# Kernel tuning notes

Measured on AMD Instinct MI355X. Metric: run time of the kernel, lower is better.

## Reference

```python
import jax, jax.numpy as jnp
import numpy as np

N_NODES = 100000
N_EDGES = 1600000
IN_DIM = 128
OUT_DIM = 64


def setup_inputs() -> dict:
    key = jax.random.key(0)
    k1, k2, k3 = jax.random.split(key, 3)
    x = jax.random.normal(k1, (N_NODES, IN_DIM), dtype=jnp.float32)
    edge_index = jax.random.randint(k2, (2, N_EDGES), 0, N_NODES, dtype=jnp.int64)
    W = jax.random.normal(k3, (IN_DIM, OUT_DIM), dtype=jnp.float32) * (1.0 / np.sqrt(IN_DIM))
    b = jnp.zeros((OUT_DIM,), dtype=jnp.float32)
    return {"x": x, "edge_index": edge_index, "W": W, "b": b}


def reference(x, edge_index, W, b):
    row = edge_index[0]  # source nodes
    col = edge_index[1]  # target nodes (aggregation index)
    n = x.shape[0]

    # gcn_norm with add_self_loops=False: degree from edge weights (ones) at target
    ones = jnp.ones((edge_index.shape[1],), dtype=x.dtype)
    deg = jax.ops.segment_sum(ones, col, num_segments=n)  # [N]
    deg_inv_sqrt = jnp.where(deg > 0, jax.lax.rsqrt(jnp.maximum(deg, 1e-12)), 0.0)
    norm = deg_inv_sqrt[row] * deg_inv_sqrt[col]  # [E]

    # linear transform first (bias added after aggregation, as in PyG GCNConv)
    h = x @ W  # [N, OUT_DIM]

    # gather source features, scale by norm, scatter-add to targets
    msg = h[row] * norm[:, None]  # [E, OUT_DIM]
    out = jax.ops.segment_sum(msg, col, num_segments=n) + b  # [N, OUT_DIM]

    return jax.nn.relu(out)
```

## Files before the change

### kernel.cpp

```cpp
#include <hip/hip_runtime.h>
#include <hip/hip_bf16.h>

#define IN_DIM 128
#define OUT_DIM 64
#define FLOG 7
#define FNPB (1 << FLOG)
#define MAXFINE 1024
#define BB 512
#define BT 512
#define EBUF_MAX 4096
#define CAP 4096
#define SPILL_MAX 65536

static inline size_t align_up(size_t v, size_t a) { return (v + a - 1) & ~(a - 1); }

__device__ __forceinline__ unsigned short f2bf(float f) {
    unsigned int x = __float_as_uint(f);
    unsigned int r = (x + 0x7fffu + ((x >> 16) & 1u)) >> 16;
    return (unsigned short)r;
}

typedef _Float16 half8 __attribute__((ext_vector_type(8)));
typedef float f32x4 __attribute__((ext_vector_type(4)));

__global__ void __launch_bounds__(BT) kAB_build(
    const int* __restrict__ row, const int* __restrict__ col,
    int* __restrict__ BinSize, unsigned int* __restrict__ EdgeBuf,
    uint2* __restrict__ spill, int* __restrict__ spillcur,
    int n_edges, int nbf, int chunk) {
    __shared__ int er[EBUF_MAX];
    __shared__ int ec[EBUF_MAX];
    __shared__ int hist[MAXFINE];
    int t = threadIdx.x;
    int start = blockIdx.x * chunk;
    int end = min(n_edges, start + chunk);
    int n = end - start;

    for (int i = t; i < nbf; i += BT) hist[i] = 0;
    __syncthreads();
    for (int i = t; i < n; i += BT) {
        int r = row[start + i];
        int c = col[start + i];
        er[i] = r;
        ec[i] = c;
        atomicAdd(&hist[c >> FLOG], 1);
    }
    __syncthreads();
    for (int i = t; i < nbf; i += BT) {
        int cv = hist[i];
        hist[i] = cv ? atomicAdd(&BinSize[i], cv) : 0;
    }
    __syncthreads();
    for (int i = t; i < n; i += BT) {
        int c = ec[i];
        int bin = c >> FLOG;
        int pos = atomicAdd(&hist[bin], 1);
        if (pos < CAP) {
            EdgeBuf[(size_t)bin * CAP + pos] =
                ((unsigned int)er[i] << FLOG) | (unsigned int)(c & (FNPB - 1));
        } else {
            int sp = atomicAdd(spillcur, 1);
            if (sp < SPILL_MAX)
                spill[sp] = make_uint2((unsigned int)er[i], (unsigned int)c);
        }
    }
}

__global__ void __launch_bounds__(256) kD_degree(
    const unsigned int* __restrict__ EdgeBuf, const int* __restrict__ BinSize,
    const uint2* __restrict__ spill, const int* __restrict__ spillcur,
    float* __restrict__ dis, int n_nodes) {
    __shared__ int cnt[FNPB];
    int t = threadIdx.x;
    int b = blockIdx.x;
    if (t < FNPB) cnt[t] = 0;
    __syncthreads();
    int sz = min(BinSize[b], CAP);
    const unsigned int* slot = EdgeBuf + (size_t)b * CAP;
    for (int i = t; i < sz; i += 256)
        atomicAdd(&cnt[slot[i] & (FNPB - 1)], 1);
    int sn = min(*spillcur, SPILL_MAX);
    for (int i = t; i < sn; i += 256) {
        uint2 e = spill[i];
        if ((int)(e.y >> FLOG) == b) atomicAdd(&cnt[e.y & (FNPB - 1)], 1);
    }
    __syncthreads();
    int node = (b << FLOG) + t;
    if (t < FNPB && node < n_nodes) {
        int d = cnt[t];
        dis[node] = (d > 0) ? rsqrtf((float)d) : 0.0f;
    }
}

__global__ void __launch_bounds__(256) k_matmul_mfma(
    const float* __restrict__ x, const float* __restrict__ W,
    const float* __restrict__ dis, unsigned short* __restrict__ h, int n_nodes) {
    const int lane = threadIdx.x & 63;
    const int m = lane & 15;
    const int q = lane >> 4;
    const int wid = (blockIdx.x * blockDim.x + threadIdx.x) >> 6;
    const int ntiles = (n_nodes + 15) >> 4;
    if (wid >= ntiles) return;

    half8 bfrag[4][4];
#pragma unroll
    for (int kt = 0; kt < 4; ++kt) {
#pragma unroll
        for (int nt = 0; nt < 4; ++nt) {
            int k0 = kt * 32 + q * 8;
            int c = nt * 16 + m;
#pragma unroll
            for (int j = 0; j < 8; ++j)
                bfrag[kt][nt][j] = (_Float16)W[(size_t)(k0 + j) * OUT_DIM + c];
        }
    }

    const int nb = wid << 4;
    int arow = nb + m;
    if (arow >= n_nodes) arow = n_nodes - 1;
    const float* xr = x + (size_t)arow * IN_DIM;

    f32x4 acc[4];
#pragma unroll
    for (int nt = 0; nt < 4; ++nt) acc[nt] = (f32x4){0.f, 0.f, 0.f, 0.f};

#pragma unroll
    for (int kt = 0; kt < 4; ++kt) {
        const float4* xp = (const float4*)(xr + kt * 32 + q * 8);
        float4 lo = xp[0];
        float4 hi = xp[1];
        half8 afrag;
        afrag[0] = (_Float16)lo.x; afrag[1] = (_Float16)lo.y;
        afrag[2] = (_Float16)lo.z; afrag[3] = (_Float16)lo.w;
        afrag[4] = (_Float16)hi.x; afrag[5] = (_Float16)hi.y;
        afrag[6] = (_Float16)hi.z; afrag[7] = (_Float16)hi.w;
#pragma unroll
        for (int nt = 0; nt < 4; ++nt)
            acc[nt] = __builtin_amdgcn_mfma_f32_16x16x32_f16(afrag, bfrag[kt][nt],
                                                             acc[nt], 0, 0, 0);
    }

#pragma unroll
    for (int r = 0; r < 4; ++r) {
        int node = nb + q * 4 + r;
        if (node < n_nodes) {
            float dv = dis[node];
            unsigned short* hp = h + (size_t)node * OUT_DIM + m;
#pragma unroll
            for (int nt = 0; nt < 4; ++nt)
                hp[nt * 16] = f2bf(acc[nt][r] * dv);
        }
    }
}

__global__ void __launch_bounds__(512) kF_sortagg(
    const unsigned int* __restrict__ EdgeBuf, const int* __restrict__ BinSize,
    const uint2* __restrict__ spill, const int* __restrict__ spillcur,
    const unsigned short* __restrict__ h, const float* __restrict__ b,
    float* __restrict__ out, int* __restrict__ arena, int* __restrict__ arenacur,
    int n_nodes) {
    __shared__ int cnt[FNPB];
    __shared__ int seg[FNPB];
    __shared__ int cursor[FNPB];
    __shared__ int sbuf[CAP];
    __shared__ int abase_sh;
    int t = threadIdx.x;
    int bk = blockIdx.x;
    int nb0 = bk << FLOG;
    int sz = min(BinSize[bk], CAP);
    const unsigned int* slot = EdgeBuf + (size_t)bk * CAP;
    int sn = min(*spillcur, SPILL_MAX);

    if (t < FNPB) cnt[t] = 0;
    __syncthreads();
    for (int i = t; i < sz; i += 512)
        atomicAdd(&cnt[slot[i] & (FNPB - 1)], 1);
    for (int i = t; i < sn; i += 512) {
        uint2 e = spill[i];
        if ((int)(e.y >> FLOG) == bk) atomicAdd(&cnt[e.y & (FNPB - 1)], 1);
    }
    __syncthreads();

    if (t < FNPB) seg[t] = cnt[t];
    __syncthreads();
    for (int off = 1; off < FNPB; off <<= 1) {
        int x = 0;
        if (t < FNPB && t >= off) x = seg[t - off];
        __syncthreads();
        if (t < FNPB) seg[t] += x;
        __syncthreads();
    }
    if (t < FNPB) cursor[t] = seg[t] - cnt[t];
    __syncthreads();

    int ne = seg[FNPB - 1];
    if (t == 0 && ne > CAP) abase_sh = atomicAdd(arenacur, ne);
    __syncthreads();

    const int lane = t & 63;
    const int wv = t >> 6;
    const int quarter = lane >> 4;
    const int qlane = lane & 15;
    float4 bias = ((const float4*)b)[qlane];

    if (ne <= CAP) {
        for (int i = t; i < sz; i += 512) {
            unsigned int v = slot[i];
            int p = atomicAdd(&cursor[v & (FNPB - 1)], 1);
            sbuf[p] = (int)(v >> FLOG);
        }
        for (int i = t; i < sn; i += 512) {
            uint2 e = spill[i];
            if ((int)(e.y >> FLOG) == bk) {
                int p = atomicAdd(&cursor[e.y & (FNPB - 1)], 1);
                sbuf[p] = (int)e.x;
            }
        }
        __syncthreads();

        for (int nl = wv; nl < FNPB; nl += 8) {
            int node = nb0 + nl;
            if (node >= n_nodes) break;
            int e_ = seg[nl];
            int dcount = cnt[nl];
            int s_ = e_ - dcount;
            float a0 = 0.f, a1 = 0.f, a2 = 0.f, a3 = 0.f;
            for (int j0 = s_; j0 < e_; j0 += 8) {
                int iA = j0 + quarter;
                int iB = j0 + quarter + 4;
                int rA = sbuf[iA < e_ ? iA : s_];
                int rB = sbuf[iB < e_ ? iB : s_];
                uint2 vA = make_uint2(0u, 0u), vB = make_uint2(0u, 0u);
                if (iA < e_)
                    vA = *(const uint2*)(h + (size_t)rA * OUT_DIM + qlane * 4);
                if (iB < e_)
                    vB = *(const uint2*)(h + (size_t)rB * OUT_DIM + qlane * 4);
                a0 += __uint_as_float(vA.x << 16);
                a1 += __uint_as_float(vA.x & 0xFFFF0000u);
                a2 += __uint_as_float(vA.y << 16);
                a3 += __uint_as_float(vA.y & 0xFFFF0000u);
                a0 += __uint_as_float(vB.x << 16);
                a1 += __uint_as_float(vB.x & 0xFFFF0000u);
                a2 += __uint_as_float(vB.y << 16);
                a3 += __uint_as_float(vB.y & 0xFFFF0000u);
            }
            a0 += __shfl_xor(a0, 16, 64); a0 += __shfl_xor(a0, 32, 64);
            a1 += __shfl_xor(a1, 16, 64); a1 += __shfl_xor(a1, 32, 64);
            a2 += __shfl_xor(a2, 16, 64); a2 += __shfl_xor(a2, 32, 64);
            a3 += __shfl_xor(a3, 16, 64); a3 += __shfl_xor(a3, 32, 64);
            if (quarter == 0) {
                float dv = (dcount > 0) ? rsqrtf((float)dcount) : 0.0f;
                float4 o;
                o.x = fmaxf(fmaf(a0, dv, bias.x), 0.f);
                o.y = fmaxf(fmaf(a1, dv, bias.y), 0.f);
                o.z = fmaxf(fmaf(a2, dv, bias.z), 0.f);
                o.w = fmaxf(fmaf(a3, dv, bias.w), 0.f);
                ((float4*)(out + (size_t)node * OUT_DIM))[qlane] = o;
            }
        }
    } else {
        int abase = abase_sh;
        for (int i = t; i < sz; i += 512) {
            unsigned int v = slot[i];
            int p = atomicAdd(&cursor[v & (FNPB - 1)], 1);
            arena[abase + p] = (int)(v >> FLOG);
        }
        for (int i = t; i < sn; i += 512) {
            uint2 e = spill[i];
            if ((int)(e.y >> FLOG) == bk) {
                int p = atomicAdd(&cursor[e.y & (FNPB - 1)], 1);
                arena[abase + p] = (int)e.x;
            }
        }
        __threadfence();
        __syncthreads();
        for (int nl = wv; nl < FNPB; nl += 8) {
            int node = nb0 + nl;
            if (node >= n_nodes) break;
            int e_ = seg[nl];
            int dcount = cnt[nl];
            int s_ = e_ - dcount;
            float a0 = 0.f, a1 = 0.f, a2 = 0.f, a3 = 0.f;
            for (int j0 = s_; j0 < e_; j0 += 8) {
                int iA = j0 + quarter;
                int iB = j0 + quarter + 4;
                int rA = arena[abase + (iA < e_ ? iA : s_)];
                int rB = arena[abase + (iB < e_ ? iB : s_)];
                uint2 vA = make_uint2(0u, 0u), vB = make_uint2(0u, 0u);
                if (iA < e_)
                    vA = *(const uint2*)(h + (size_t)rA * OUT_DIM + qlane * 4);
                if (iB < e_)
                    vB = *(const uint2*)(h + (size_t)rB * OUT_DIM + qlane * 4);
                a0 += __uint_as_float(vA.x << 16);
                a1 += __uint_as_float(vA.x & 0xFFFF0000u);
                a2 += __uint_as_float(vA.y << 16);
                a3 += __uint_as_float(vA.y & 0xFFFF0000u);
                a0 += __uint_as_float(vB.x << 16);
                a1 += __uint_as_float(vB.x & 0xFFFF0000u);
                a2 += __uint_as_float(vB.y << 16);
                a3 += __uint_as_float(vB.y & 0xFFFF0000u);
            }
            a0 += __shfl_xor(a0, 16, 64); a0 += __shfl_xor(a0, 32, 64);
            a1 += __shfl_xor(a1, 16, 64); a1 += __shfl_xor(a1, 32, 64);
            a2 += __shfl_xor(a2, 16, 64); a2 += __shfl_xor(a2, 32, 64);
            a3 += __shfl_xor(a3, 16, 64); a3 += __shfl_xor(a3, 32, 64);
            if (quarter == 0) {
                float dv = (dcount > 0) ? rsqrtf((float)dcount) : 0.0f;
                float4 o;
                o.x = fmaxf(fmaf(a0, dv, bias.x), 0.f);
                o.y = fmaxf(fmaf(a1, dv, bias.y), 0.f);
                o.z = fmaxf(fmaf(a2, dv, bias.z), 0.f);
                o.w = fmaxf(fmaf(a3, dv, bias.w), 0.f);
                ((float4*)(out + (size_t)node * OUT_DIM))[qlane] = o;
            }
        }
    }
}

#define MM_NODES 16
__global__ void __launch_bounds__(256) k_matmul_f32(
    const float* __restrict__ x, const float* __restrict__ W,
    const float* __restrict__ dis, float* __restrict__ h, int n_nodes) {
    __shared__ float xs[MM_NODES * IN_DIM];
    const int lane = threadIdx.x & 63;
    const int wv = threadIdx.x >> 6;
    float w[IN_DIM];
#pragma unroll
    for (int k = 0; k < IN_DIM; ++k) w[k] = W[k * OUT_DIM + lane];
    int nchunks = (n_nodes + MM_NODES - 1) / MM_NODES;
    for (int ch = blockIdx.x; ch < nchunks; ch += gridDim.x) {
        int base = ch * MM_NODES;
        int nrows = min(MM_NODES, n_nodes - base);
        __syncthreads();
        const float4* xg = (const float4*)(x + (size_t)base * IN_DIM);
        int nf4 = nrows * IN_DIM / 4;
        for (int i = threadIdx.x; i < nf4; i += 256) ((float4*)xs)[i] = xg[i];
        __syncthreads();
#pragma unroll
        for (int j = 0; j < 4; ++j) {
            int local = wv * 4 + j;
            int node = base + local;
            if (local < nrows) {
                const float4* xr = (const float4*)(xs + local * IN_DIM);
                float acc = 0.0f;
#pragma unroll
                for (int k4 = 0; k4 < IN_DIM / 4; ++k4) {
                    float4 xv = xr[k4];
                    acc = fmaf(xv.x, w[k4 * 4 + 0], acc);
                    acc = fmaf(xv.y, w[k4 * 4 + 1], acc);
                    acc = fmaf(xv.z, w[k4 * 4 + 2], acc);
                    acc = fmaf(xv.w, w[k4 * 4 + 3], acc);
                }
                h[(size_t)node * OUT_DIM + lane] = acc * dis[node];
            }
        }
    }
}

__global__ void k_degree_fb(const int* __restrict__ col, int* __restrict__ deg,
                            int n_edges) {
    int i = blockIdx.x * blockDim.x + threadIdx.x;
    int stride = gridDim.x * blockDim.x;
    for (; i < n_edges; i += stride) atomicAdd(&deg[col[i]], 1);
}

__global__ void k_rsqrt_fb(const int* __restrict__ deg, float* __restrict__ dis, int n) {
    int i = blockIdx.x * blockDim.x + threadIdx.x;
    if (i < n) {
        int d = deg[i];
        dis[i] = (d > 0) ? rsqrtf((float)d) : 0.0f;
    }
}

__global__ void __launch_bounds__(256) k_scatter_fb(
    const int* __restrict__ row, const int* __restrict__ col,
    const float* __restrict__ dis, const float* __restrict__ h,
    float* __restrict__ out, int n_edges) {
    const int lane = threadIdx.x & 63;
    int e = (blockIdx.x * blockDim.x + threadIdx.x) >> 6;
    int nw = (gridDim.x * blockDim.x) >> 6;
    for (; e < n_edges; e += nw) {
        int r = row[e];
        int c = col[e];
        float v = h[(size_t)r * OUT_DIM + lane] * dis[c];
        atomicAdd(&out[(size_t)c * OUT_DIM + lane], v);
    }
}

__global__ void k_bias_relu_fb(float* __restrict__ out, const float* __restrict__ b,
                               int total) {
    int i = blockIdx.x * blockDim.x + threadIdx.x;
    int stride = gridDim.x * blockDim.x;
    for (; i < total; i += stride) {
        float v = out[i] + b[i & (OUT_DIM - 1)];
        out[i] = fmaxf(v, 0.0f);
    }
}

extern "C" void kernel_launch(void* const* d_in, const int* in_sizes, int n_in,
                              void* d_out, int out_size, void* d_ws, size_t ws_size,
                              hipStream_t stream) {
    const float* x = (const float*)d_in[0];
    const int* ei = (const int*)d_in[1];
    const float* W = (const float*)d_in[2];
    const float* b = (const float*)d_in[3];
    float* out = (float*)d_out;

    const int n_nodes = in_sizes[0] / IN_DIM;
    const int n_edges = in_sizes[1] / 2;
    const int* row = ei;
    const int* col = ei + n_edges;

    const int nbf = (n_nodes + FNPB - 1) >> FLOG;
    const int chunk = (n_edges + BB - 1) / BB;

    char* wsb = (char*)d_ws;
    size_t off = 0;
    int* BinSize = (int*)(wsb + off);    off += (size_t)(nbf + 8) * 4;
    int* spillcur = BinSize + nbf;
    int* arenacur = BinSize + nbf + 1;
    const size_t zero_bytes = off;
    off = align_up(off, 256);
    unsigned int* EdgeBuf = (unsigned int*)(wsb + off);
                                         off += align_up((size_t)nbf * CAP * 4, 256);
    uint2* spill = (uint2*)(wsb + off);  off += align_up((size_t)SPILL_MAX * 8, 256);
    int* arena = (int*)(wsb + off);      off += align_up((size_t)n_edges * 4, 256);
    float* dis = (float*)(wsb + off);    off += align_up((size_t)n_nodes * 4, 256);
    unsigned short* h = (unsigned short*)(wsb + off);
                                         off += (size_t)n_nodes * OUT_DIM * 2;
    const size_t needed = off;

    const bool ok = (ws_size >= needed) && (nbf <= MAXFINE) &&
                    (chunk <= EBUF_MAX) && (n_nodes <= (1 << 24));

    if (ok) {
        hipMemsetAsync(BinSize, 0, zero_bytes, stream);
        kAB_build<<<BB, BT, 0, stream>>>(row, col, BinSize, EdgeBuf, spill,
                                         spillcur, n_edges, nbf, chunk);
        kD_degree<<<nbf, 256, 0, stream>>>(EdgeBuf, BinSize, spill, spillcur,
                                           dis, n_nodes);
        int ntiles = (n_nodes + 15) / 16;
        int mm_blocks = (ntiles + 3) / 4;
        k_matmul_mfma<<<mm_blocks, 256, 0, stream>>>(x, W, dis, h, n_nodes);
        kF_sortagg<<<nbf, 512, 0, stream>>>(EdgeBuf, BinSize, spill, spillcur,
                                            h, b, out, arena, arenacur, n_nodes);
    } else {
        char* p = (char*)d_ws;
        int* deg_f = (int*)p;
        float* dis_f = (float*)(p + align_up((size_t)n_nodes * 4, 256));
        float* h_f = (float*)(p + 2 * align_up((size_t)n_nodes * 4, 256));
        hipMemsetAsync(deg_f, 0, (size_t)n_nodes * 4, stream);
        hipMemsetAsync(out, 0, (size_t)out_size * 4, stream);
        k_degree_fb<<<1024, 256, 0, stream>>>(col, deg_f, n_edges);
        k_rsqrt_fb<<<(n_nodes + 255) / 256, 256, 0, stream>>>(deg_f, dis_f, n_nodes);
        k_matmul_f32<<<1024, 256, 0, stream>>>(x, W, dis_f, h_f, n_nodes);
        k_scatter_fb<<<2048, 256, 0, stream>>>(row, col, dis_f, h_f, out, n_edges);
        k_bias_relu_fb<<<2048, 256, 0, stream>>>(out, b, n_nodes * OUT_DIM);
    }
}
```

Measured before the change: 180.5 us.

## Fuse edge binning with matmul and apply source normalization during aggregation

Merges the edge-bucketing kernel and the MFMA matmul into one launch, with extra blocks that run the matmul concurrently with binning. This is possible because the matmul no longer scales by the source degree normalization. That scaling moves into the aggregation loop, which now gathers dis[row] per edge and uses FMA. The build kernel also keeps edge indices in registers instead of shared memory. The aim is to overlap the dense matmul with the atomic-heavy binning and drop a kernel boundary, at the cost of an extra random gather per edge in aggregation.

New measurement: 181.4 us. About the same (+0.5%).

```diff
diff --git a/kernel.cpp b/kernel.cpp
--- a/kernel.cpp
+++ b/kernel.cpp
@@ -8,7 +8,7 @@
 #define MAXFINE 1024
 #define BB 512
 #define BT 512
-#define EBUF_MAX 4096
+#define MAXE 8
 #define CAP 4096
 #define SPILL_MAX 65536
 
@@ -23,45 +23,115 @@
 typedef _Float16 half8 __attribute__((ext_vector_type(8)));
 typedef float f32x4 __attribute__((ext_vector_type(4)));
 
-__global__ void __launch_bounds__(BT) kAB_build(
+__global__ void __launch_bounds__(BT, 4) k_build_mm(
     const int* __restrict__ row, const int* __restrict__ col,
     int* __restrict__ BinSize, unsigned int* __restrict__ EdgeBuf,
     uint2* __restrict__ spill, int* __restrict__ spillcur,
-    int n_edges, int nbf, int chunk) {
-    __shared__ int er[EBUF_MAX];
-    __shared__ int ec[EBUF_MAX];
-    __shared__ int hist[MAXFINE];
-    int t = threadIdx.x;
-    int start = blockIdx.x * chunk;
-    int end = min(n_edges, start + chunk);
-    int n = end - start;
-
-    for (int i = t; i < nbf; i += BT) hist[i] = 0;
-    __syncthreads();
-    for (int i = t; i < n; i += BT) {
-        int r = row[start + i];
-        int c = col[start + i];
-        er[i] = r;
-        ec[i] = c;
-        atomicAdd(&hist[c >> FLOG], 1);
-    }
-    __syncthreads();
-    for (int i = t; i < nbf; i += BT) {
-        int cv = hist[i];
-        hist[i] = cv ? atomicAdd(&BinSize[i], cv) : 0;
-    }
-    __syncthreads();
-    for (int i = t; i < n; i += BT) {
-        int c = ec[i];
-        int bin = c >> FLOG;
-        int pos = atomicAdd(&hist[bin], 1);
-        if (pos < CAP) {
-            EdgeBuf[(size_t)bin * CAP + pos] =
-                ((unsigned int)er[i] << FLOG) | (unsigned int)(c & (FNPB - 1));
-        } else {
-            int sp = atomicAdd(spillcur, 1);
-            if (sp < SPILL_MAX)
-                spill[sp] = make_uint2((unsigned int)er[i], (unsigned int)c);
+    const float* __restrict__ x, const float* __restrict__ W,
+    unsigned short* __restrict__ h,
+    int n_edges, int n_nodes, int nbf, int chunk, int mm_blocks) {
+    if ((int)blockIdx.x < BB) {
+        __shared__ int hist[MAXFINE];
+        int t = threadIdx.x;
+        int start = blockIdx.x * chunk;
+        int end = min(n_edges, start + chunk);
+        int n = end - start;
+
+        for (int i = t; i < nbf; i += BT) hist[i] = 0;
+        __syncthreads();
+
+        int er[MAXE], ec[MAXE];
+#pragma unroll
+        for (int u = 0; u < MAXE; ++u) {
+            int i = t + u * BT;
+            ec[u] = -1;
+            if (i < n) {
+                er[u] = row[start + i];
+                int c = col[start + i];
+                ec[u] = c;
+                atomicAdd(&hist[c >> FLOG], 1);
+            }
+        }
+        __syncthreads();
+        for (int i = t; i < nbf; i += BT) {
+            int cv = hist[i];
+            hist[i] = cv ? atomicAdd(&BinSize[i], cv) : 0;
+        }
+        __syncthreads();
+#pragma unroll
+        for (int u = 0; u < MAXE; ++u) {
+            int c = ec[u];
+            if (c >= 0) {
+                int bin = c >> FLOG;
+                int pos = atomicAdd(&hist[bin], 1);
+                if (pos < CAP) {
+                    EdgeBuf[(size_t)bin * CAP + pos] =
+                        ((unsigned int)er[u] << FLOG) | (unsigned int)(c & (FNPB - 1));
+                } else {
+                    int sp = atomicAdd(spillcur, 1);
+                    if (sp < SPILL_MAX)
+                        spill[sp] = make_uint2((unsigned int)er[u], (unsigned int)c);
+                }
+            }
+        }
+    } else {
+        const int lane = threadIdx.x & 63;
+        const int m = lane & 15;
+        const int q = lane >> 4;
+        const int wv = threadIdx.x >> 6;
+        const int wid0 = ((int)blockIdx.x - BB) * 8 + wv;
+        const int nwaves = mm_blocks * 8;
+        const int ntiles = (n_nodes + 15) >> 4;
+
+        half8 bfrag[4][4];
+#pragma unroll
+        for (int kt = 0; kt < 4; ++kt) {
+#pragma unroll
+            for (int nt = 0; nt < 4; ++nt) {
+                int k0 = kt * 32 + q * 8;
+                int c = nt * 16 + m;
+#pragma unroll
+                for (int j = 0; j < 8; ++j)
+                    bfrag[kt][nt][j] = (_Float16)W[(size_t)(k0 + j) * OUT_DIM + c];
+            }
+        }
+
+        for (int wid = wid0; wid < ntiles; wid += nwaves) {
+            const int nb = wid << 4;
+            int arow = nb + m;
+            if (arow >= n_nodes) arow = n_nodes - 1;
+            const float* xr = x + (size_t)arow * IN_DIM;
+
+            f32x4 acc[4];
+#pragma unroll
+            for (int nt = 0; nt < 4; ++nt) acc[nt] = (f32x4){0.f, 0.f, 0.f, 0.f};
+
+#pragma unroll
+            for (int kt = 0; kt < 4; ++kt) {
+                const float4* xp = (const float4*)(xr + kt * 32 + q * 8);
+                float4 lo = xp[0];
+                float4 hi = xp[1];
+                half8 afrag;
+                afrag[0] = (_Float16)lo.x; afrag[1] = (_Float16)lo.y;
+                afrag[2] = (_Float16)lo.z; afrag[3] = (_Float16)lo.w;
+                afrag[4] = (_Float16)hi.x; afrag[5] = (_Float16)hi.y;
+                afrag[6] = (_Float16)hi.z; afrag[7] = (_Float16)hi.w;
+#pragma unroll
+                for (int nt = 0; nt < 4; ++nt)
+                    acc[nt] = __builtin_amdgcn_mfma_f32_16x16x32_f16(
+                        afrag, bfrag[kt][nt], acc[nt], 0, 0, 0);
+            }
+
+#pragma unroll
+            for (int r = 0; r < 4; ++r) {
+                int node = nb + q * 4 + r;
+                if (node < n_nodes) {
+                    unsigned short* hp = h + (size_t)node * OUT_DIM + m;
+#pragma unroll
+                    for (int nt = 0; nt < 4; ++nt)
+                        hp[nt * 16] = f2bf(acc[nt][r]);
+                }
+            }
         }
     }
 }
@@ -92,71 +162,11 @@
     }
 }
 
-__global__ void __launch_bounds__(256) k_matmul_mfma(
-    const float* __restrict__ x, const float* __restrict__ W,
-    const float* __restrict__ dis, unsigned short* __restrict__ h, int n_nodes) {
-    const int lane = threadIdx.x & 63;
-    const int m = lane & 15;
-    const int q = lane >> 4;
-    const int wid = (blockIdx.x * blockDim.x + threadIdx.x) >> 6;
-    const int ntiles = (n_nodes + 15) >> 4;
-    if (wid >= ntiles) return;
-
-    half8 bfrag[4][4];
-#pragma unroll
-    for (int kt = 0; kt < 4; ++kt) {
-#pragma unroll
-        for (int nt = 0; nt < 4; ++nt) {
-            int k0 = kt * 32 + q * 8;
-            int c = nt * 16 + m;
-#pragma unroll
-            for (int j = 0; j < 8; ++j)
-                bfrag[kt][nt][j] = (_Float16)W[(size_t)(k0 + j) * OUT_DIM + c];
-        }
-    }
-
-    const int nb = wid << 4;
-    int arow = nb + m;
-    if (arow >= n_nodes) arow = n_nodes - 1;
-    const float* xr = x + (size_t)arow * IN_DIM;
-
-    f32x4 acc[4];
-#pragma unroll
-    for (int nt = 0; nt < 4; ++nt) acc[nt] = (f32x4){0.f, 0.f, 0.f, 0.f};
-
-#pragma unroll
-    for (int kt = 0; kt < 4; ++kt) {
-        const float4* xp = (const float4*)(xr + kt * 32 + q * 8);
-        float4 lo = xp[0];
-        float4 hi = xp[1];
-        half8 afrag;
-        afrag[0] = (_Float16)lo.x; afrag[1] = (_Float16)lo.y;
-        afrag[2] = (_Float16)lo.z; afrag[3] = (_Float16)lo.w;
-        afrag[4] = (_Float16)hi.x; afrag[5] = (_Float16)hi.y;
-        afrag[6] = (_Float16)hi.z; afrag[7] = (_Float16)hi.w;
-#pragma unroll
-        for (int nt = 0; nt < 4; ++nt)
-            acc[nt] = __builtin_amdgcn_mfma_f32_16x16x32_f16(afrag, bfrag[kt][nt],
-                                                             acc[nt], 0, 0, 0);
-    }
-
-#pragma unroll
-    for (int r = 0; r < 4; ++r) {
-        int node = nb + q * 4 + r;
-        if (node < n_nodes) {
-            float dv = dis[node];
-            unsigned short* hp = h + (size_t)node * OUT_DIM + m;
-#pragma unroll
-            for (int nt = 0; nt < 4; ++nt)
-                hp[nt * 16] = f2bf(acc[nt][r] * dv);
-        }
-    }
-}
-
 __global__ void __launch_bounds__(512) kF_sortagg(
     const unsigned int* __restrict__ EdgeBuf, const int* __restrict__ BinSize,
     const uint2* __restrict__ spill, const int* __restrict__ spillcur,
-    const unsigned short* __restrict__ h, const float* __restrict__ b,
+    const unsigned short* __restrict__ h, const float* __restrict__ dis,
+    const float* __restrict__ b,
     float* __restrict__ out, int* __restrict__ arena, int* __restrict__ arenacur,
     int n_nodes) {
     __shared__ int cnt[FNPB];
@@ -230,19 +240,21 @@
                 int iB = j0 + quarter + 4;
                 int rA = sbuf[iA < e_ ? iA : s_];
                 int rB = sbuf[iB < e_ ? iB : s_];
+                float dA = dis[rA];
+                float dB = dis[rB];
                 uint2 vA = make_uint2(0u, 0u), vB = make_uint2(0u, 0u);
                 if (iA < e_)
                     vA = *(const uint2*)(h + (size_t)rA * OUT_DIM + qlane * 4);
                 if (iB < e_)
                     vB = *(const uint2*)(h + (size_t)rB * OUT_DIM + qlane * 4);
-                a0 += __uint_as_float(vA.x << 16);
-                a1 += __uint_as_float(vA.x & 0xFFFF0000u);
-                a2 += __uint_as_float(vA.y << 16);
-                a3 += __uint_as_float(vA.y & 0xFFFF0000u);
-                a0 += __uint_as_float(vB.x << 16);
-                a1 += __uint_as_float(vB.x & 0xFFFF0000u);
-                a2 += __uint_as_float(vB.y << 16);
-                a3 += __uint_as_float(vB.y & 0xFFFF0000u);
+                a0 = fmaf(__uint_as_float(vA.x << 16), dA, a0);
+                a1 = fmaf(__uint_as_float(vA.x & 0xFFFF0000u), dA, a1);
+                a2 = fmaf(__uint_as_float(vA.y << 16), dA, a2);
+                a3 = fmaf(__uint_as_float(vA.y & 0xFFFF0000u), dA, a3);
+                a0 = fmaf(__uint_as_float(vB.x << 16), dB, a0);
+                a1 = fmaf(__uint_as_float(vB.x & 0xFFFF0000u), dB, a1);
+                a2 = fmaf(__uint_as_float(vB.y << 16), dB, a2);
+                a3 = fmaf(__uint_as_float(vB.y & 0xFFFF0000u), dB, a3);
             }
             a0 += __shfl_xor(a0, 16, 64); a0 += __shfl_xor(a0, 32, 64);
             a1 += __shfl_xor(a1, 16, 64); a1 += __shfl_xor(a1, 32, 64);
@@ -286,19 +298,21 @@
                 int iB = j0 + quarter + 4;
                 int rA = arena[abase + (iA < e_ ? iA : s_)];
                 int rB = arena[abase + (iB < e_ ? iB : s_)];
+                float dA = dis[rA];
+                float dB = dis[rB];
                 uint2 vA = make_uint2(0u, 0u), vB = make_uint2(0u, 0u);
                 if (iA < e_)
                     vA = *(const uint2*)(h + (size_t)rA * OUT_DIM + qlane * 4);
                 if (iB < e_)
                     vB = *(const uint2*)(h + (size_t)rB * OUT_DIM + qlane * 4);
-                a0 += __uint_as_float(vA.x << 16);
-                a1 += __uint_as_float(vA.x & 0xFFFF0000u);
-                a2 += __uint_as_float(vA.y << 16);
-                a3 += __uint_as_float(vA.y & 0xFFFF0000u);
-                a0 += __uint_as_float(vB.x << 16);
-                a1 += __uint_as_float(vB.x & 0xFFFF0000u);
-                a2 += __uint_as_float(vB.y << 16);
-                a3 += __uint_as_float(vB.y & 0xFFFF0000u);
+                a0 = fmaf(__uint_as_float(vA.x << 16), dA, a0);
+                a1 = fmaf(__uint_as_float(vA.x & 0xFFFF0000u), dA, a1);
+                a2 = fmaf(__uint_as_float(vA.y << 16), dA, a2);
+                a3 = fmaf(__uint_as_float(vA.y & 0xFFFF0000u), dA, a3);
+                a0 = fmaf(__uint_as_float(vB.x << 16), dB, a0);
+                a1 = fmaf(__uint_as_float(vB.x & 0xFFFF0000u), dB, a1);
+                a2 = fmaf(__uint_as_float(vB.y << 16), dB, a2);
+                a3 = fmaf(__uint_as_float(vB.y & 0xFFFF0000u), dB, a3);
             }
             a0 += __shfl_xor(a0, 16, 64); a0 += __shfl_xor(a0, 32, 64);
             a1 += __shfl_xor(a1, 16, 64); a1 += __shfl_xor(a1, 32, 64);
@@ -431,19 +445,21 @@
     const size_t needed = off;
 
     const bool ok = (ws_size >= needed) && (nbf <= MAXFINE) &&
-                    (chunk <= EBUF_MAX) && (n_nodes <= (1 << 24));
+                    (chunk <= MAXE * BT) && (n_nodes <= (1 << 24));
 
     if (ok) {
+        const int ntiles = (n_nodes + 15) >> 4;
+        int mm_blocks = (ntiles + 15) / 16;
+        if (mm_blocks < 1) mm_blocks = 1;
         hipMemsetAsync(BinSize, 0, zero_bytes, stream);
-        kAB_build<<<BB, BT, 0, stream>>>(row, col, BinSize, EdgeBuf, spill,
-                                         spillcur, n_edges, nbf, chunk);
+        k_build_mm<<<BB + mm_blocks, BT, 0, stream>>>(
+            row, col, BinSize, EdgeBuf, spill, spillcur,
+            x, W, h, n_edges, n_nodes, nbf, chunk, mm_blocks);
         kD_degree<<<nbf, 256, 0, stream>>>(EdgeBuf, BinSize, spill, spillcur,
                                            dis, n_nodes);
-        int ntiles = (n_nodes + 15) / 16;
-        int mm_blocks = (ntiles + 3) / 4;
-        k_matmul_mfma<<<mm_blocks, 256, 0, stream>>>(x, W, dis, h, n_nodes);
         kF_sortagg<<<nbf, 512, 0, stream>>>(EdgeBuf, BinSize, spill, spillcur,
-                                            h, b, out, arena, arenacur, n_nodes);
+                                            h, dis, b, out, arena, arenacur,
+                                            n_nodes);
     } else {
         char* p = (char*)d_ws;
         int* deg_f = (int*)p;
```
